# Kernel optimization log

Hardware: AMD Instinct MI355X
Metric: run time of the kernel (lower is better)

Reference implementation:

```python
import jax, jax.numpy as jnp
import numpy as np

H = 1024
V = 50257
S = 8192


def setup_inputs() -> dict:
    key = jax.random.key(0)
    ks = jax.random.split(key, 13)
    s = 0.02  # param init scale
    return {
        "input": jax.random.randint(ks[0], (1,), 0, V),
        "hidden": jax.random.normal(ks[1], (1, 1, H), jnp.float32),
        "encoder_outputs": jax.random.normal(ks[2], (S, H), jnp.float32),
        "embedding": jax.random.normal(ks[3], (V, H), jnp.float32) * s,
        "attn_w": jax.random.normal(ks[4], (1, 2 * H), jnp.float32) * s,
        "attn_b": jnp.zeros((1,), jnp.float32),
        "comb_w": jax.random.normal(ks[5], (H, 2 * H), jnp.float32) * s,
        "comb_b": jnp.zeros((H,), jnp.float32),
        "w_ih": jax.random.normal(ks[6], (3 * H, H), jnp.float32) * s,
        "w_hh": jax.random.normal(ks[7], (3 * H, H), jnp.float32) * s,
        "b_ih": jnp.zeros((3 * H,), jnp.float32),
        "b_hh": jnp.zeros((3 * H,), jnp.float32),
        "out_w": jax.random.normal(ks[8], (V, H), jnp.float32) * s,
        "out_b": jnp.zeros((V,), jnp.float32),
    }


def reference(input, hidden, encoder_outputs, embedding, attn_w, attn_b,
              comb_w, comb_b, w_ih, w_hh, b_ih, b_hh, out_w, out_b):
    # embedded = embedding(input).view(1,1,-1); dropout in eval mode = identity
    emb = embedding[input[0]]            # [H]
    h0 = hidden[0, 0]                    # [H]
    # Original loop computes the SAME score attn(cat(emb, hidden)) for every
    # timestep -> softmax over a constant vector (uniform weights). Compute the
    # scalar once and broadcast (same math, one GEMV instead of S launches).
    score = jnp.concatenate([emb, h0]) @ attn_w[0] + attn_b[0]   # scalar
    seq_len = encoder_outputs.shape[0]
    attn_weights = jax.nn.softmax(jnp.broadcast_to(score, (seq_len,)))  # [S]
    attn_applied = attn_weights @ encoder_outputs                # [H]
    combined = jnp.concatenate([emb, attn_applied]) @ comb_w.T + comb_b  # [H]
    x = jax.nn.relu(combined)
    # Single GRU step (torch nn.GRU gate math)
    gi = w_ih @ x + b_ih                 # [3H]
    gh = w_hh @ h0 + b_hh                # [3H]
    i_r, i_z, i_n = jnp.split(gi, 3)
    h_r, h_z, h_n = jnp.split(gh, 3)
    r = jax.nn.sigmoid(i_r + h_r)
    z = jax.nn.sigmoid(i_z + h_z)
    n = jnp.tanh(i_n + r * h_n)
    h_new = (1.0 - z) * n + z * h0       # [H]
    logits = h_new @ out_w.T + out_b     # [V]
    output = jax.nn.log_softmax(logits)[None, :]   # [1, V]
    return output, h_new[None, None, :], attn_weights[None, :]
```

## Files before the change

kernel.cpp:

```cpp
#include <hip/hip_runtime.h>
#include <math.h>

#define HN 1024
#define VN 50257
#define SN 8192

#define WS_PARTIAL 0
#define WS_AA      262144
#define WS_X       263168
#define WS_GH      264192
#define WS_CEMB    267264
#define WS_HNEW    270336
#define WS_LOGITS  271360
#define WS_EXPD    321618

__device__ __forceinline__ float wred(float v) {
#pragma unroll
  for (int m = 32; m; m >>= 1) v += __shfl_xor(v, m);
  return v;
}

__device__ __forceinline__ float dot4(float4 a, float4 b) {
  return a.x * b.x + a.y * b.y + a.z * b.z + a.w * b.w;
}

__global__ __launch_bounds__(1024) void k1_front(
    const float* __restrict__ enc, const float* __restrict__ w_hh,
    const float* __restrict__ hidden, const int* __restrict__ token,
    const float* __restrict__ embedding, const float* __restrict__ comb_w,
    const float* __restrict__ comb_b, float* __restrict__ ws,
    float* __restrict__ out_attn) {
  const int blk = blockIdx.x, t = threadIdx.x;
  if (blk < 256) {
    __shared__ float4 lds[1024];
    const int g = t >> 8, c4 = t & 255;
    const float4* e4 = (const float4*)enc + ((size_t)blk * 32 + g * 8) * 256 + c4;
    float4 acc = make_float4(0.f, 0.f, 0.f, 0.f);
#pragma unroll
    for (int r = 0; r < 8; ++r) {
      float4 v = e4[r * 256];
      acc.x += v.x; acc.y += v.y; acc.z += v.z; acc.w += v.w;
    }
    lds[t] = acc;
    __syncthreads();
    if (t < 256) {
      float4 a = lds[t], b = lds[t + 256], c = lds[t + 512], d = lds[t + 768];
      float4 s = make_float4(a.x + b.x + c.x + d.x, a.y + b.y + c.y + d.y,
                             a.z + b.z + c.z + d.z, a.w + b.w + c.w + d.w);
      ((float4*)(ws + WS_PARTIAL))[blk * 256 + t] = s;
    }
    if (t < 32) out_attn[blk * 32 + t] = 1.f / 8192.f;
  } else if (blk < 352) {
    const int wg = (blk - 256) * 16 + (t >> 6);
    const int l = t & 63;
    const float4* h4 = (const float4*)hidden;
    float4 hv0 = h4[l], hv1 = h4[64 + l], hv2 = h4[128 + l], hv3 = h4[192 + l];
#pragma unroll
    for (int k = 0; k < 2; ++k) {
      const int r = wg + k * 1536;
      const float4* m4 = (const float4*)w_hh + (size_t)r * 256;
      float acc = dot4(m4[l], hv0) + dot4(m4[64 + l], hv1) +
                  dot4(m4[128 + l], hv2) + dot4(m4[192 + l], hv3);
      acc = wred(acc);
      if (l == 0) ws[WS_GH + r] = acc;
    }
  } else {
    const int iw = (blk - 352) * 16 + (t >> 6);
    const int l = t & 63;
    const int tok = token[0];
    const float4* emb4 = (const float4*)embedding + (size_t)tok * 256;
#pragma unroll
    for (int k = 0; k < 2; ++k) {
      const int i = iw + k * 512;
      const float4* cw4 = (const float4*)comb_w + (size_t)i * 512;
      float acc = dot4(cw4[l], emb4[l]) + dot4(cw4[64 + l], emb4[64 + l]) +
                  dot4(cw4[128 + l], emb4[128 + l]) + dot4(cw4[192 + l], emb4[192 + l]);
      acc = wred(acc);
      if (l == 0) ws[WS_CEMB + i] = acc + comb_b[i];
    }
  }
}

__global__ __launch_bounds__(1024) void k2_reduce(float* __restrict__ ws) {
  __shared__ float lds[1024];
  const int t = threadIdx.x, b = blockIdx.x;
  const int c = b * 32 + (t & 31), rg = t >> 5;
  const float* p = ws + WS_PARTIAL;
  float s = 0.f;
#pragma unroll
  for (int j = 0; j < 8; ++j) s += p[(rg * 8 + j) * 1024 + c];
  lds[t] = s;
  __syncthreads();
  if (t < 32) {
    float a = 0.f;
#pragma unroll
    for (int j = 0; j < 32; ++j) a += lds[j * 32 + t];
    ws[WS_AA + b * 32 + t] = a * (1.f / 8192.f);
  }
}

__global__ void k3_x(const float* __restrict__ comb_w, float* __restrict__ ws) {
  const int w = threadIdx.x >> 6, l = threadIdx.x & 63;
  const int i = blockIdx.x * 4 + w;
  const float4* aa4 = (const float4*)(ws + WS_AA);
  const float4* cw4 = (const float4*)comb_w + (size_t)i * 512 + 256;
  float acc = dot4(cw4[l], aa4[l]) + dot4(cw4[64 + l], aa4[64 + l]) +
              dot4(cw4[128 + l], aa4[128 + l]) + dot4(cw4[192 + l], aa4[192 + l]);
  acc = wred(acc);
  if (l == 0) ws[WS_X + i] = fmaxf(ws[WS_CEMB + i] + acc, 0.f);
}

__global__ void k4_gates_h(const float* __restrict__ w_ih,
                           const float* __restrict__ b_ih, const float* __restrict__ b_hh,
                           const float* __restrict__ hidden, float* __restrict__ ws,
                           float* __restrict__ d_out) {
  const int w = threadIdx.x >> 6, l = threadIdx.x & 63;
  const int i = blockIdx.x * 4 + w;
  const float4* x4 = (const float4*)(ws + WS_X);
  float4 xv0 = x4[l], xv1 = x4[64 + l], xv2 = x4[128 + l], xv3 = x4[192 + l];
  const float4* m0 = (const float4*)w_ih + (size_t)i * 256;
  const float4* m1 = (const float4*)w_ih + (size_t)(i + 1024) * 256;
  const float4* m2 = (const float4*)w_ih + (size_t)(i + 2048) * 256;
  float a0 = dot4(m0[l], xv0) + dot4(m0[64 + l], xv1) +
             dot4(m0[128 + l], xv2) + dot4(m0[192 + l], xv3);
  float a1 = dot4(m1[l], xv0) + dot4(m1[64 + l], xv1) +
             dot4(m1[128 + l], xv2) + dot4(m1[192 + l], xv3);
  float a2 = dot4(m2[l], xv0) + dot4(m2[64 + l], xv1) +
             dot4(m2[128 + l], xv2) + dot4(m2[192 + l], xv3);
  a0 = wred(a0); a1 = wred(a1); a2 = wred(a2);
  if (l == 0) {
    float ir = a0 + b_ih[i];
    float iz = a1 + b_ih[i + 1024];
    float inn = a2 + b_ih[i + 2048];
    float hr = ws[WS_GH + i] + b_hh[i];
    float hz = ws[WS_GH + i + 1024] + b_hh[i + 1024];
    float hn = ws[WS_GH + i + 2048] + b_hh[i + 2048];
    float rg = 1.f / (1.f + expf(-(ir + hr)));
    float zg = 1.f / (1.f + expf(-(iz + hz)));
    float ng = tanhf(inn + rg * hn);
    float h = (1.f - zg) * ng + zg * hidden[i];
    ws[WS_HNEW + i] = h;
    d_out[VN + i] = h;
  }
}

__global__ void k5_logits(const float* __restrict__ out_w, const float* __restrict__ out_b,
                          float* __restrict__ ws) {
  const int blk = blockIdx.x, t = threadIdx.x;
  const int w = t >> 6, l = t & 63;
  const int gw = blk * 4 + w;
  __shared__ float4 hs4[256];
  __shared__ double sd[4];
  hs4[t] = ((const float4*)(ws + WS_HNEW))[t];
  __syncthreads();
  float4 h0_ = hs4[l], h1_ = hs4[64 + l], h2_ = hs4[128 + l], h3_ = hs4[192 + l];
  const float4* ow4 = (const float4*)out_w;
  double eacc = 0.0;
#pragma unroll
  for (int it = 0; it < 3; ++it) {
    const int v0 = gw + it * 16896;
    const int v1 = v0 + 8448;
    const bool ok1 = (v1 < VN);
    const float4* r0 = ow4 + (size_t)v0 * 256;
    const float4* r1 = ow4 + (size_t)(ok1 ? v1 : v0) * 256;
    float a0 = dot4(r0[l], h0_) + dot4(r0[64 + l], h1_) +
               dot4(r0[128 + l], h2_) + dot4(r0[192 + l], h3_);
    float a1 = dot4(r1[l], h0_) + dot4(r1[64 + l], h1_) +
               dot4(r1[128 + l], h2_) + dot4(r1[192 + l], h3_);
    a0 = wred(a0);
    a1 = wred(a1);
    if (l == 0) {
      float lg0 = a0 + out_b[v0];
      ws[WS_LOGITS + v0] = lg0;
      eacc += (double)expf(lg0);
      if (ok1) {
        float lg1 = a1 + out_b[v1];
        ws[WS_LOGITS + v1] = lg1;
        eacc += (double)expf(lg1);
      }
    }
  }
  if (l == 0) sd[w] = eacc;
  __syncthreads();
  if (t == 0) ((double*)(ws + WS_EXPD))[blk] = sd[0] + sd[1] + sd[2] + sd[3];
}

__global__ void k6_final(const float* __restrict__ ws, float* __restrict__ d_out) {
  __shared__ double sd[256];
  const int t = threadIdx.x;
  const double* ed = (const double*)(ws + WS_EXPD);
  double a = 0.0;
#pragma unroll
  for (int j = 0; j < 8; ++j) a += ed[t + j * 256];
  if (t < 64) a += ed[t + 2048];
  sd[t] = a;
  __syncthreads();
  for (int s = 128; s; s >>= 1) {
    if (t < s) sd[t] += sd[t + s];
    __syncthreads();
  }
  const float logZ = (float)log(sd[0]);
  const int v = blockIdx.x * 256 + t;
  if (v < VN) d_out[v] = ws[WS_LOGITS + v] - logZ;
}

extern "C" void kernel_launch(void* const* d_in, const int* in_sizes, int n_in,
                              void* d_out, int out_size, void* d_ws, size_t ws_size,
                              hipStream_t stream) {
  const int* token = (const int*)d_in[0];
  const float* hidden = (const float*)d_in[1];
  const float* enc = (const float*)d_in[2];
  const float* embedding = (const float*)d_in[3];
  const float* comb_w = (const float*)d_in[6];
  const float* comb_b = (const float*)d_in[7];
  const float* w_ih = (const float*)d_in[8];
  const float* w_hh = (const float*)d_in[9];
  const float* b_ih = (const float*)d_in[10];
  const float* b_hh = (const float*)d_in[11];
  const float* out_w = (const float*)d_in[12];
  const float* out_b = (const float*)d_in[13];
  float* out = (float*)d_out;
  float* ws = (float*)d_ws;

  k1_front<<<384, 1024, 0, stream>>>(enc, w_hh, hidden, token, embedding,
                                     comb_w, comb_b, ws, out + VN + HN);
  k2_reduce<<<32, 1024, 0, stream>>>(ws);
  k3_x<<<256, 256, 0, stream>>>(comb_w, ws);
  k4_gates_h<<<256, 256, 0, stream>>>(w_ih, b_ih, b_hh, hidden, ws, out);
  k5_logits<<<2112, 256, 0, stream>>>(out_w, out_b, ws);
  k6_final<<<197, 256, 0, stream>>>(ws, out);
}
```

Baseline: 60.16 us.

## Merge front-kernel roles into every block and batch logits rows per wave

The front kernel now has every one of 256 blocks sum its slice of encoder_outputs and then use its 16 waves for 12 w_hh rows plus 4 comb_w embedding rows, instead of splitting work across 384 specialized blocks. The logits kernel drops the LDS staging of h_new and its barrier, reads h_new straight from global memory, and issues three independent row dot-products per group in two groups rather than two per iteration in three iterations. The aim is more loads in flight per wave and an even balance of work across blocks. The cost is more register pressure in the logits kernel and a longer critical path per front block.

```diff
diff --git a/kernel.cpp b/kernel.cpp
--- a/kernel.cpp
+++ b/kernel.cpp
@@ -31,8 +31,8 @@
     const float* __restrict__ comb_b, float* __restrict__ ws,
     float* __restrict__ out_attn) {
   const int blk = blockIdx.x, t = threadIdx.x;
-  if (blk < 256) {
-    __shared__ float4 lds[1024];
+  __shared__ float4 lds[1024];
+  {
     const int g = t >> 8, c4 = t & 255;
     const float4* e4 = (const float4*)enc + ((size_t)blk * 32 + g * 8) * 256 + c4;
     float4 acc = make_float4(0.f, 0.f, 0.f, 0.f);
@@ -42,42 +42,33 @@
       acc.x += v.x; acc.y += v.y; acc.z += v.z; acc.w += v.w;
     }
     lds[t] = acc;
-    __syncthreads();
-    if (t < 256) {
-      float4 a = lds[t], b = lds[t + 256], c = lds[t + 512], d = lds[t + 768];
-      float4 s = make_float4(a.x + b.x + c.x + d.x, a.y + b.y + c.y + d.y,
-                             a.z + b.z + c.z + d.z, a.w + b.w + c.w + d.w);
-      ((float4*)(ws + WS_PARTIAL))[blk * 256 + t] = s;
-    }
-    if (t < 32) out_attn[blk * 32 + t] = 1.f / 8192.f;
-  } else if (blk < 352) {
-    const int wg = (blk - 256) * 16 + (t >> 6);
-    const int l = t & 63;
+  }
+  __syncthreads();
+  if (t < 256) {
+    float4 a = lds[t], b = lds[t + 256], c = lds[t + 512], d = lds[t + 768];
+    float4 s = make_float4(a.x + b.x + c.x + d.x, a.y + b.y + c.y + d.y,
+                           a.z + b.z + c.z + d.z, a.w + b.w + c.w + d.w);
+    ((float4*)(ws + WS_PARTIAL))[blk * 256 + t] = s;
+  }
+  if (t < 32) out_attn[blk * 32 + t] = 1.f / 8192.f;
+  const int w = t >> 6, l = t & 63;
+  if (w < 12) {
+    const int r = blk * 12 + w;
     const float4* h4 = (const float4*)hidden;
-    float4 hv0 = h4[l], hv1 = h4[64 + l], hv2 = h4[128 + l], hv3 = h4[192 + l];
-#pragma unroll
-    for (int k = 0; k < 2; ++k) {
-      const int r = wg + k * 1536;
-      const float4* m4 = (const float4*)w_hh + (size_t)r * 256;
-      float acc = dot4(m4[l], hv0) + dot4(m4[64 + l], hv1) +
-                  dot4(m4[128 + l], hv2) + dot4(m4[192 + l], hv3);
-      acc = wred(acc);
-      if (l == 0) ws[WS_GH + r] = acc;
-    }
+    const float4* m4 = (const float4*)w_hh + (size_t)r * 256;
+    float acc = dot4(m4[l], h4[l]) + dot4(m4[64 + l], h4[64 + l]) +
+                dot4(m4[128 + l], h4[128 + l]) + dot4(m4[192 + l], h4[192 + l]);
+    acc = wred(acc);
+    if (l == 0) ws[WS_GH + r] = acc;
   } else {
-    const int iw = (blk - 352) * 16 + (t >> 6);
-    const int l = t & 63;
+    const int i = blk * 4 + (w - 12);
     const int tok = token[0];
     const float4* emb4 = (const float4*)embedding + (size_t)tok * 256;
-#pragma unroll
-    for (int k = 0; k < 2; ++k) {
-      const int i = iw + k * 512;
-      const float4* cw4 = (const float4*)comb_w + (size_t)i * 512;
-      float acc = dot4(cw4[l], emb4[l]) + dot4(cw4[64 + l], emb4[64 + l]) +
-                  dot4(cw4[128 + l], emb4[128 + l]) + dot4(cw4[192 + l], emb4[192 + l]);
-      acc = wred(acc);
-      if (l == 0) ws[WS_CEMB + i] = acc + comb_b[i];
-    }
+    const float4* cw4 = (const float4*)comb_w + (size_t)i * 512;
+    float acc = dot4(cw4[l], emb4[l]) + dot4(cw4[64 + l], emb4[64 + l]) +
+                dot4(cw4[128 + l], emb4[128 + l]) + dot4(cw4[192 + l], emb4[192 + l]);
+    acc = wred(acc);
+    if (l == 0) ws[WS_CEMB + i] = acc + comb_b[i];
   }
 }
 
@@ -149,37 +140,59 @@
   const int blk = blockIdx.x, t = threadIdx.x;
   const int w = t >> 6, l = t & 63;
   const int gw = blk * 4 + w;
-  __shared__ float4 hs4[256];
-  __shared__ double sd[4];
-  hs4[t] = ((const float4*)(ws + WS_HNEW))[t];
-  __syncthreads();
-  float4 h0_ = hs4[l], h1_ = hs4[64 + l], h2_ = hs4[128 + l], h3_ = hs4[192 + l];
+  const float4* h4p = (const float4*)(ws + WS_HNEW);
+  float4 h0_ = h4p[l], h1_ = h4p[64 + l], h2_ = h4p[128 + l], h3_ = h4p[192 + l];
   const float4* ow4 = (const float4*)out_w;
   double eacc = 0.0;
-#pragma unroll
-  for (int it = 0; it < 3; ++it) {
-    const int v0 = gw + it * 16896;
-    const int v1 = v0 + 8448;
-    const bool ok1 = (v1 < VN);
+  {
+    const int v0 = gw, v1 = gw + 8448, v2 = gw + 16896;
     const float4* r0 = ow4 + (size_t)v0 * 256;
-    const float4* r1 = ow4 + (size_t)(ok1 ? v1 : v0) * 256;
+    const float4* r1 = ow4 + (size_t)v1 * 256;
+    const float4* r2 = ow4 + (size_t)v2 * 256;
     float a0 = dot4(r0[l], h0_) + dot4(r0[64 + l], h1_) +
                dot4(r0[128 + l], h2_) + dot4(r0[192 + l], h3_);
     float a1 = dot4(r1[l], h0_) + dot4(r1[64 + l], h1_) +
                dot4(r1[128 + l], h2_) + dot4(r1[192 + l], h3_);
-    a0 = wred(a0);
-    a1 = wred(a1);
+    float a2 = dot4(r2[l], h0_) + dot4(r2[64 + l], h1_) +
+               dot4(r2[128 + l], h2_) + dot4(r2[192 + l], h3_);
+    a0 = wred(a0); a1 = wred(a1); a2 = wred(a2);
     if (l == 0) {
       float lg0 = a0 + out_b[v0];
+      float lg1 = a1 + out_b[v1];
+      float lg2 = a2 + out_b[v2];
       ws[WS_LOGITS + v0] = lg0;
-      eacc += (double)expf(lg0);
-      if (ok1) {
-        float lg1 = a1 + out_b[v1];
-        ws[WS_LOGITS + v1] = lg1;
-        eacc += (double)expf(lg1);
+      ws[WS_LOGITS + v1] = lg1;
+      ws[WS_LOGITS + v2] = lg2;
+      eacc += (double)expf(lg0) + (double)expf(lg1) + (double)expf(lg2);
+    }
+  }
+  {
+    const int v0 = gw + 25344, v1 = gw + 33792, v2 = gw + 42240;
+    const bool ok2 = (v2 < VN);
+    const float4* r0 = ow4 + (size_t)v0 * 256;
+    const float4* r1 = ow4 + (size_t)v1 * 256;
+    const float4* r2 = ow4 + (size_t)(ok2 ? v2 : v1) * 256;
+    float a0 = dot4(r0[l], h0_) + dot4(r0[64 + l], h1_) +
+               dot4(r0[128 + l], h2_) + dot4(r0[192 + l], h3_);
+    float a1 = dot4(r1[l], h0_) + dot4(r1[64 + l], h1_) +
+               dot4(r1[128 + l], h2_) + dot4(r1[192 + l], h3_);
+    float a2 = dot4(r2[l], h0_) + dot4(r2[64 + l], h1_) +
+               dot4(r2[128 + l], h2_) + dot4(r2[192 + l], h3_);
+    a0 = wred(a0); a1 = wred(a1); a2 = wred(a2);
+    if (l == 0) {
+      float lg0 = a0 + out_b[v0];
+      float lg1 = a1 + out_b[v1];
+      ws[WS_LOGITS + v0] = lg0;
+      ws[WS_LOGITS + v1] = lg1;
+      eacc += (double)expf(lg0) + (double)expf(lg1);
+      if (ok2) {
+        float lg2 = a2 + out_b[v2];
+        ws[WS_LOGITS + v2] = lg2;
+        eacc += (double)expf(lg2);
       }
     }
   }
+  __shared__ double sd[4];
   if (l == 0) sd[w] = eacc;
   __syncthreads();
   if (t == 0) ((double*)(ws + WS_EXPD))[blk] = sd[0] + sd[1] + sd[2] + sd[3];
@@ -222,7 +235,7 @@
   float* out = (float*)d_out;
   float* ws = (float*)d_ws;
 
-  k1_front<<<384, 1024, 0, stream>>>(enc, w_hh, hidden, token, embedding,
+  k1_front<<<256, 1024, 0, stream>>>(enc, w_hh, hidden, token, embedding,
                                      comb_w, comb_b, ws, out + VN + HN);
   k2_reduce<<<32, 1024, 0, stream>>>(ws);
   k3_x<<<256, 256, 0, stream>>>(comb_w, ws);
```

After: 58.16 us. 3.3% less time.
